# Performance work log

Hardware: AMD Instinct MI355X
Metric: run time of the kernel (lower is better)

## Reference

```python
import jax, jax.numpy as jnp
import numpy as np

N_NODES = 50000


def _gin_conv(x, src, dst, w1, b1, w2, b2):
    # sum-aggregate neighbor features: agg[i] = sum_{(j->i) in E} x[j]
    agg = jax.ops.segment_sum(x[src], dst, num_segments=N_NODES)
    h = x + agg  # eps = 0 (PyG GINConv default, not trainable)
    h = jnp.maximum(h @ w1 + b1, 0.0) @ w2 + b2
    return h


def setup_inputs() -> dict:
    key = jax.random.key(0)
    ks = jax.random.split(key, 10)
    d_in, d_h, d_out = 128, 256, 2
    E = 600000
    x = jax.random.normal(ks[0], (N_NODES, d_in), dtype=jnp.float32)
    edge_index = jax.random.randint(ks[1], (2, E), 0, N_NODES, dtype=jnp.int64)
    s = lambda k, sh: jax.random.normal(k, sh, dtype=jnp.float32) * (1.0 / np.sqrt(sh[0]))
    return {
        "x": x,
        "edge_index": edge_index,
        "w1": s(ks[2], (d_in, d_h)), "b1": jnp.zeros((d_h,), jnp.float32),
        "w2": s(ks[3], (d_h, d_h)), "b2": jnp.zeros((d_h,), jnp.float32),
        "w3": s(ks[4], (d_h, d_h)), "b3": jnp.zeros((d_h,), jnp.float32),
        "w4": s(ks[5], (d_h, d_out)), "b4": jnp.zeros((d_out,), jnp.float32),
    }


def reference(x, edge_index, w1, b1, w2, b2, w3, b3, w4, b4):
    src, dst = edge_index[0], edge_index[1]
    h = _gin_conv(x, src, dst, w1, b1, w2, b2)
    h = jnp.maximum(h, 0.0)  # F.relu between the two GINConv layers
    h = _gin_conv(h, src, dst, w3, b3, w4, b4)
    return jax.nn.log_softmax(h, axis=1)
```

## Files before the change

### kernel.cpp

```cpp
#include <hip/hip_runtime.h>
#include <hip/hip_bf16.h>


typedef __attribute__((ext_vector_type(8))) short bf16x8;
typedef __attribute__((ext_vector_type(4))) float f32x4;

static __device__ __forceinline__ unsigned short f2bf(float f) {
    unsigned int u = __float_as_uint(f);
    unsigned int r = (u + 0x7fffu + ((u >> 16) & 1u)) >> 16;
    return (unsigned short)r;
}
static __device__ __forceinline__ float bf2f(unsigned short s) {
    return __uint_as_float(((unsigned int)s) << 16);
}
static __device__ __forceinline__ float bflo(unsigned int u) {
    return __uint_as_float(u << 16);
}
static __device__ __forceinline__ float bfhi(unsigned int u) {
    return __uint_as_float(u & 0xffff0000u);
}

#define S1 136
#define S2 264

__global__ __launch_bounds__(256) void degree_kernel(
    const int* __restrict__ dst, int* __restrict__ deg, int E)
{
    const int e = blockIdx.x * 256 + threadIdx.x;
    if (e < E) atomicAdd(&deg[dst[e]], 1);
}

__global__ __launch_bounds__(256) void block_sum_kernel(
    const int* __restrict__ deg, int* __restrict__ bsum, int M)
{
    const int b = blockIdx.x, t = threadIdx.x;
    const int idx = b * 1024 + t * 4;
    int s = 0;
    if (idx + 3 < M) {
        const int4 v = *(const int4*)(deg + idx);
        s = v.x + v.y + v.z + v.w;
    } else {
        #pragma unroll
        for (int i = 0; i < 4; ++i) if (idx + i < M) s += deg[idx + i];
    }
    #pragma unroll
    for (int off = 32; off > 0; off >>= 1) s += __shfl_down(s, off);
    __shared__ int ws[4];
    if ((t & 63) == 0) ws[t >> 6] = s;
    __syncthreads();
    if (t == 0) bsum[b] = ws[0] + ws[1] + ws[2] + ws[3];
}

__global__ __launch_bounds__(64) void scan_partials_kernel(
    const int* __restrict__ bsum, int* __restrict__ boff, int nB)
{
    const int t = threadIdx.x;
    const int v = (t < nB) ? bsum[t] : 0;
    int inc = v;
    #pragma unroll
    for (int off = 1; off < 64; off <<= 1) {
        const int u = __shfl_up(inc, off);
        if (t >= off) inc += u;
    }
    if (t < nB) boff[t] = inc - v;
}

__global__ __launch_bounds__(256) void scan_blocks_kernel(
    const int* __restrict__ deg, const int* __restrict__ boff,
    int* __restrict__ rowptr, int* __restrict__ cur, int M, int E)
{
    const int b = blockIdx.x, t = threadIdx.x;
    const int idx = b * 1024 + t * 4;
    int4 d = make_int4(0, 0, 0, 0);
    if (idx + 3 < M) {
        d = *(const int4*)(deg + idx);
    } else {
        if (idx + 0 < M) d.x = deg[idx + 0];
        if (idx + 1 < M) d.y = deg[idx + 1];
        if (idx + 2 < M) d.z = deg[idx + 2];
        if (idx + 3 < M) d.w = deg[idx + 3];
    }
    const int tot = d.x + d.y + d.z + d.w;
    const int lane = t & 63, wid = t >> 6;
    int inc = tot;
    #pragma unroll
    for (int off = 1; off < 64; off <<= 1) {
        const int u = __shfl_up(inc, off);
        if (lane >= off) inc += u;
    }
    __shared__ int wsum[4];
    if (lane == 63) wsum[wid] = inc;
    __syncthreads();
    int woff = 0;
    #pragma unroll
    for (int w = 0; w < 4; ++w) if (w < wid) woff += wsum[w];
    int p = boff[b] + woff + (inc - tot);
    if (idx + 0 < M) { rowptr[idx + 0] = p; cur[idx + 0] = p; } p += d.x;
    if (idx + 1 < M) { rowptr[idx + 1] = p; cur[idx + 1] = p; } p += d.y;
    if (idx + 2 < M) { rowptr[idx + 2] = p; cur[idx + 2] = p; } p += d.z;
    if (idx + 3 < M) { rowptr[idx + 3] = p; cur[idx + 3] = p; }
    if (b == 0 && t == 0) rowptr[M] = E;
}

__global__ __launch_bounds__(256) void fill_kernel(
    const int* __restrict__ src, const int* __restrict__ dst,
    int* __restrict__ cur, int* __restrict__ srcs, int E)
{
    const int e = blockIdx.x * 256 + threadIdx.x;
    if (e >= E) return;
    const int p = atomicAdd(&cur[dst[e]], 1);
    srcs[p] = src[e];
}

__global__ __launch_bounds__(256) void cvt_bf16_kernel(
    const float* __restrict__ in, short* __restrict__ outb, int n4)
{
    const int i = (blockIdx.x * 256 + threadIdx.x);
    if (i >= n4) return;
    const float4 v = *(const float4*)(in + (size_t)i * 4);
    ushort4 o;
    o.x = f2bf(v.x); o.y = f2bf(v.y); o.z = f2bf(v.z); o.w = f2bf(v.w);
    *(ushort4*)(outb + (size_t)i * 4) = o;
}

__global__ __launch_bounds__(256) void transpose_cvt3_kernel(
    const float* __restrict__ w1, const float* __restrict__ w2, const float* __restrict__ w3,
    short* __restrict__ w1t, short* __restrict__ w2t, short* __restrict__ w3t)
{
    const int z = blockIdx.z;
    const float* in; short* outb; int K, ostride;
    if (z == 0)      { in = w1; outb = w1t; K = 128; ostride = S1; }
    else if (z == 1) { in = w2; outb = w2t; K = 256; ostride = S2; }
    else             { in = w3; outb = w3t; K = 256; ostride = S2; }
    const int N = 256;
    const int k0 = blockIdx.x * 32;
    if (k0 >= K) return;
    const int n0 = blockIdx.y * 32;
    __shared__ float tile[32][33];
    const int tx = threadIdx.x & 31;
    const int ty = threadIdx.x >> 5;
    #pragma unroll
    for (int i = 0; i < 4; ++i)
        tile[ty + 8 * i][tx] = in[(size_t)(k0 + ty + 8 * i) * N + n0 + tx];
    __syncthreads();
    #pragma unroll
    for (int i = 0; i < 4; ++i)
        outb[(size_t)(n0 + ty + 8 * i) * ostride + k0 + tx] = (short)f2bf(tile[tx][ty + 8 * i]);
}

__global__ __launch_bounds__(256) void gather_add_d128(
    const short* __restrict__ feat,
    const int* __restrict__ rowptr, const int* __restrict__ srcs,
    short* __restrict__ outb, int M)
{
    const int row = blockIdx.x * 4 + (threadIdx.x >> 6);
    if (row >= M) return;
    const int o = (threadIdx.x & 63) * 2;
    const unsigned int u = *(const unsigned int*)(feat + (size_t)row * 128 + o);
    float a0 = bflo(u), a1 = bfhi(u);
    const int jb = rowptr[row], je = rowptr[row + 1];
    int j = jb;
    for (; j + 8 <= je; j += 8) {
        unsigned int v[8];
        #pragma unroll
        for (int t = 0; t < 8; ++t) {
            const int s = srcs[j + t];
            v[t] = *(const unsigned int*)(feat + (size_t)s * 128 + o);
        }
        #pragma unroll
        for (int t = 0; t < 8; ++t) { a0 += bflo(v[t]); a1 += bfhi(v[t]); }
    }
    if (j + 4 <= je) {
        unsigned int v[4];
        #pragma unroll
        for (int t = 0; t < 4; ++t) {
            const int s = srcs[j + t];
            v[t] = *(const unsigned int*)(feat + (size_t)s * 128 + o);
        }
        #pragma unroll
        for (int t = 0; t < 4; ++t) { a0 += bflo(v[t]); a1 += bfhi(v[t]); }
        j += 4;
    }
    for (; j < je; ++j) {
        const unsigned int v = *(const unsigned int*)(feat + (size_t)srcs[j] * 128 + o);
        a0 += bflo(v); a1 += bfhi(v);
    }
    const unsigned int up = (unsigned int)f2bf(a0) | ((unsigned int)f2bf(a1) << 16);
    *(unsigned int*)(outb + (size_t)row * S1 + o) = up;
}

__global__ __launch_bounds__(256) void gather_add_d256(
    const short* __restrict__ feat,
    const int* __restrict__ rowptr, const int* __restrict__ srcs,
    short* __restrict__ outb, int M)
{
    const int row = blockIdx.x * 4 + (threadIdx.x >> 6);
    if (row >= M) return;
    const int o = (threadIdx.x & 63) * 4;
    const uint2 u = *(const uint2*)(feat + (size_t)row * 256 + o);
    float a0 = bflo(u.x), a1 = bfhi(u.x);
    float a2 = bflo(u.y), a3 = bfhi(u.y);
    const int jb = rowptr[row], je = rowptr[row + 1];
    int j = jb;
    for (; j + 8 <= je; j += 8) {
        uint2 v[8];
        #pragma unroll
        for (int t = 0; t < 8; ++t) {
            const int s = srcs[j + t];
            v[t] = *(const uint2*)(feat + (size_t)s * 256 + o);
        }
        #pragma unroll
        for (int t = 0; t < 8; ++t) {
            a0 += bflo(v[t].x); a1 += bfhi(v[t].x);
            a2 += bflo(v[t].y); a3 += bfhi(v[t].y);
        }
    }
    if (j + 4 <= je) {
        uint2 v[4];
        #pragma unroll
        for (int t = 0; t < 4; ++t) {
            const int s = srcs[j + t];
            v[t] = *(const uint2*)(feat + (size_t)s * 256 + o);
        }
        #pragma unroll
        for (int t = 0; t < 4; ++t) {
            a0 += bflo(v[t].x); a1 += bfhi(v[t].x);
            a2 += bflo(v[t].y); a3 += bfhi(v[t].y);
        }
        j += 4;
    }
    for (; j < je; ++j) {
        const uint2 v = *(const uint2*)(feat + (size_t)srcs[j] * 256 + o);
        a0 += bflo(v.x); a1 += bfhi(v.x); a2 += bflo(v.y); a3 += bfhi(v.y);
    }
    uint2 up;
    up.x = (unsigned int)f2bf(a0) | ((unsigned int)f2bf(a1) << 16);
    up.y = (unsigned int)f2bf(a2) | ((unsigned int)f2bf(a3) << 16);
    *(uint2*)(outb + (size_t)row * S2 + o) = up;
}

__global__ __launch_bounds__(256) void layer1_fused(
    const short* __restrict__ h1in,
    const short* __restrict__ w1t,
    const float* __restrict__ b1,
    const short* __restrict__ w2t,
    const float* __restrict__ b2,
    short* __restrict__ h1,
    int M)
{
    __shared__ short sT[64 * S2];
    const int tid  = threadIdx.x;
    const int lane = tid & 63;
    const int wid  = tid >> 6;
    const int r16  = lane & 15;
    const int q    = lane >> 4;
    const int tm   = blockIdx.x * 64;
    const int wn   = wid * 64;

    f32x4 acc[4][4];
    #pragma unroll
    for (int i = 0; i < 4; ++i)
        #pragma unroll
        for (int j = 0; j < 4; ++j)
            acc[i][j] = (f32x4)0.f;

    const short* Abase = h1in + (size_t)tm * S1;
    #pragma unroll
    for (int k0 = 0; k0 < 128; k0 += 32) {
        bf16x8 af[4], bfr[4];
        #pragma unroll
        for (int i = 0; i < 4; ++i)
            af[i] = *(const bf16x8*)(Abase + (size_t)(i * 16 + r16) * S1 + k0 + q * 8);
        #pragma unroll
        for (int j = 0; j < 4; ++j)
            bfr[j] = *(const bf16x8*)(w1t + (size_t)(wn + j * 16 + r16) * S1 + k0 + q * 8);
        #pragma unroll
        for (int i = 0; i < 4; ++i)
            #pragma unroll
            for (int j = 0; j < 4; ++j)
                acc[i][j] = __builtin_amdgcn_mfma_f32_16x16x32_bf16(af[i], bfr[j], acc[i][j], 0, 0, 0);
    }

    #pragma unroll
    for (int j = 0; j < 4; ++j) {
        const int col = wn + j * 16 + r16;
        const float bj = b1[col];
        #pragma unroll
        for (int i = 0; i < 4; ++i)
            #pragma unroll
            for (int r = 0; r < 4; ++r) {
                float v = fmaxf(acc[i][j][r] + bj, 0.f);
                sT[(i * 16 + q * 4 + r) * S2 + col] = (short)f2bf(v);
            }
    }
    __syncthreads();

    #pragma unroll
    for (int i = 0; i < 4; ++i)
        #pragma unroll
        for (int j = 0; j < 4; ++j)
            acc[i][j] = (f32x4)0.f;

    #pragma unroll
    for (int k0 = 0; k0 < 256; k0 += 32) {
        bf16x8 af[4], bfr[4];
        #pragma unroll
        for (int i = 0; i < 4; ++i)
            af[i] = *(const bf16x8*)(&sT[(i * 16 + r16) * S2 + k0 + q * 8]);
        #pragma unroll
        for (int j = 0; j < 4; ++j)
            bfr[j] = *(const bf16x8*)(w2t + (size_t)(wn + j * 16 + r16) * S2 + k0 + q * 8);
        #pragma unroll
        for (int i = 0; i < 4; ++i)
            #pragma unroll
            for (int j = 0; j < 4; ++j)
                acc[i][j] = __builtin_amdgcn_mfma_f32_16x16x32_bf16(af[i], bfr[j], acc[i][j], 0, 0, 0);
    }
    __syncthreads();

    #pragma unroll
    for (int j = 0; j < 4; ++j) {
        const int col = wn + j * 16 + r16;
        const float bj = b2[col];
        #pragma unroll
        for (int i = 0; i < 4; ++i)
            #pragma unroll
            for (int r = 0; r < 4; ++r) {
                float v = fmaxf(acc[i][j][r] + bj, 0.f);
                sT[(i * 16 + q * 4 + r) * S2 + col] = (short)f2bf(v);
            }
    }
    __syncthreads();

    #pragma unroll
    for (int c = 0; c < 8; ++c) {
        const int idx = tid + c * 256;
        const int row = idx >> 5;
        const int ch  = idx & 31;
        const int rg  = tm + row;
        if (rg < M) {
            const uint4 v = *(const uint4*)(&sT[row * S2 + ch * 8]);
            *(uint4*)(h1 + (size_t)rg * 256 + ch * 8) = v;
        }
    }
}

__global__ __launch_bounds__(256) void layer2_fused(
    const short* __restrict__ h2in,
    const short* __restrict__ w3t,
    const float* __restrict__ b3,
    const float* __restrict__ w4,
    const float* __restrict__ b4,
    float* __restrict__ out,
    int M)
{
    __shared__ short sT[64 * S2];
    const int tid  = threadIdx.x;
    const int lane = tid & 63;
    const int wid  = tid >> 6;
    const int r16  = lane & 15;
    const int q    = lane >> 4;
    const int tm   = blockIdx.x * 64;
    const int wn   = wid * 64;

    f32x4 acc[4][4];
    #pragma unroll
    for (int i = 0; i < 4; ++i)
        #pragma unroll
        for (int j = 0; j < 4; ++j)
            acc[i][j] = (f32x4)0.f;

    const short* Abase = h2in + (size_t)tm * S2;
    #pragma unroll
    for (int k0 = 0; k0 < 256; k0 += 32) {
        bf16x8 af[4], bfr[4];
        #pragma unroll
        for (int i = 0; i < 4; ++i)
            af[i] = *(const bf16x8*)(Abase + (size_t)(i * 16 + r16) * S2 + k0 + q * 8);
        #pragma unroll
        for (int j = 0; j < 4; ++j)
            bfr[j] = *(const bf16x8*)(w3t + (size_t)(wn + j * 16 + r16) * S2 + k0 + q * 8);
        #pragma unroll
        for (int i = 0; i < 4; ++i)
            #pragma unroll
            for (int j = 0; j < 4; ++j)
                acc[i][j] = __builtin_amdgcn_mfma_f32_16x16x32_bf16(af[i], bfr[j], acc[i][j], 0, 0, 0);
    }

    #pragma unroll
    for (int j = 0; j < 4; ++j) {
        const int col = wn + j * 16 + r16;
        const float bj = b3[col];
        #pragma unroll
        for (int i = 0; i < 4; ++i)
            #pragma unroll
            for (int r = 0; r < 4; ++r) {
                float v = fmaxf(acc[i][j][r] + bj, 0.f);
                sT[(i * 16 + q * 4 + r) * S2 + col] = (short)f2bf(v);
            }
    }
    __syncthreads();

    const int row = tid >> 2;
    const int qd  = tid & 3;
    const short* tp = &sT[row * S2 + qd * 64];
    const float* w4p = w4 + qd * 128;
    float s0 = 0.f, s1 = 0.f;
    #pragma unroll 8
    for (int k = 0; k < 64; ++k) {
        const float a = bf2f((unsigned short)tp[k]);
        const float2 w = *(const float2*)(w4p + 2 * k);
        s0 = fmaf(a, w.x, s0);
        s1 = fmaf(a, w.y, s1);
    }
    s0 += __shfl_down(s0, 2, 4);  s1 += __shfl_down(s1, 2, 4);
    s0 += __shfl_down(s0, 1, 4);  s1 += __shfl_down(s1, 1, 4);
    if (qd == 0) {
        const int rg = tm + row;
        if (rg < M) {
            s0 += b4[0];
            s1 += b4[1];
            const float m = fmaxf(s0, s1);
            const float l = logf(__expf(s0 - m) + __expf(s1 - m));
            float2 o;
            o.x = s0 - m - l;
            o.y = s1 - m - l;
            *(float2*)(out + (size_t)rg * 2) = o;
        }
    }
}

extern "C" void kernel_launch(void* const* d_in, const int* in_sizes, int n_in,
                              void* d_out, int out_size, void* d_ws, size_t ws_size,
                              hipStream_t stream)
{
    const float* x  = (const float*)d_in[0];
    const int*   ei = (const int*)d_in[1];
    const float* w1 = (const float*)d_in[2];
    const float* b1 = (const float*)d_in[3];
    const float* w2 = (const float*)d_in[4];
    const float* b2 = (const float*)d_in[5];
    const float* w3 = (const float*)d_in[6];
    const float* b3 = (const float*)d_in[7];
    const float* w4 = (const float*)d_in[8];
    const float* b4 = (const float*)d_in[9];

    const int DIN = 128, DH = 256;
    const int M = in_sizes[0] / DIN;
    const int E = in_sizes[1] / 2;
    const int* src = ei;
    const int* dst = ei + E;
    const int nB = (M + 1023) / 1024;

    int* deg    = (int*)d_ws;
    int* cur    = deg + M;
    int* rowptr = cur + M;
    int* bsum   = rowptr + (M + 1);
    int* boff   = bsum + 64;
    int* srcs   = boff + 64;
    size_t off = ((size_t)(3 * M + 1 + 128 + E) * sizeof(int) + 255) & ~(size_t)255;
    short* x_bf = (short*)((char*)d_ws + off);  off += (size_t)M * DIN * 2;
    off = (off + 255) & ~(size_t)255;
    short* h1in = (short*)((char*)d_ws + off);  off += (size_t)M * S1 * 2;
    off = (off + 255) & ~(size_t)255;
    short* h1   = (short*)((char*)d_ws + off);  off += (size_t)M * DH * 2;
    off = (off + 255) & ~(size_t)255;
    short* h2in = (short*)((char*)d_ws + off);  off += (size_t)M * S2 * 2;
    off = (off + 255) & ~(size_t)255;
    short* w1t  = (short*)((char*)d_ws + off);  off += (size_t)DH * S1 * 2;
    off = (off + 255) & ~(size_t)255;
    short* w2t  = (short*)((char*)d_ws + off);  off += (size_t)DH * S2 * 2;
    off = (off + 255) & ~(size_t)255;
    short* w3t  = (short*)((char*)d_ws + off);  off += (size_t)DH * S2 * 2;

    hipMemsetAsync(deg, 0, (size_t)M * sizeof(int), stream);
    degree_kernel<<<(E + 255) / 256, 256, 0, stream>>>(dst, deg, E);
    block_sum_kernel<<<nB, 256, 0, stream>>>(deg, bsum, M);
    scan_partials_kernel<<<1, 64, 0, stream>>>(bsum, boff, nB);
    scan_blocks_kernel<<<nB, 256, 0, stream>>>(deg, boff, rowptr, cur, M, E);
    fill_kernel<<<(E + 255) / 256, 256, 0, stream>>>(src, dst, cur, srcs, E);

    cvt_bf16_kernel<<<((M * DIN / 4) + 255) / 256, 256, 0, stream>>>(x, x_bf, M * DIN / 4);
    transpose_cvt3_kernel<<<dim3(8, 8, 3), 256, 0, stream>>>(w1, w2, w3, w1t, w2t, w3t);

    const int nblk = (M + 63) / 64;

    gather_add_d128<<<(M + 3) / 4, 256, 0, stream>>>(x_bf, rowptr, srcs, h1in, M);
    layer1_fused<<<nblk, 256, 0, stream>>>(h1in, w1t, b1, w2t, b2, h1, M);

    gather_add_d256<<<(M + 3) / 4, 256, 0, stream>>>(h1, rowptr, srcs, h2in, M);
    layer2_fused<<<nblk, 256, 0, stream>>>(h2in, w3t, b3, w4, b4, (float*)d_out, M);
}
```

Measured before the change: 289.0 us.

## Merge prep kernels, fold partial scan, and split gather across half-wavefronts

The memset, x-to-bf16 conversion and weight transpose are merged into one launch, and the block-offset scan is folded into the scan-blocks kernel, so the pipeline issues fewer kernel launches. Both gather kernels now split each wavefront into two halves that walk alternate neighbors with wider vector loads, then combine the halves with a cross-lane shuffle. This raises the number of neighbor loads in flight and the bytes per load, at the cost of extra registers and a reduction step. The new prep kernel's __syncthreads sits after early returns, but it only runs in the uniformly-branching transpose blocks.

```diff
diff --git a/kernel.cpp b/kernel.cpp
--- a/kernel.cpp
+++ b/kernel.cpp
@@ -22,6 +22,59 @@
 
 #define S1 136
 #define S2 264
+
+__global__ __launch_bounds__(256) void prep_kernel(
+    const float* __restrict__ x, short* __restrict__ x_bf,
+    const float* __restrict__ w1, const float* __restrict__ w2, const float* __restrict__ w3,
+    short* __restrict__ w1t, short* __restrict__ w2t, short* __restrict__ w3t,
+    int* __restrict__ deg, int M, int zB, int cB)
+{
+    const int b = blockIdx.x;
+    const int t = threadIdx.x;
+    if (b < zB) {
+        const int idx = b * 1024 + t * 4;
+        if (idx + 3 < M) {
+            *(int4*)(deg + idx) = make_int4(0, 0, 0, 0);
+        } else {
+            #pragma unroll
+            for (int i = 0; i < 4; ++i) if (idx + i < M) deg[idx + i] = 0;
+        }
+        return;
+    }
+    if (b < zB + cB) {
+        const int i = (b - zB) * 256 + t;
+        const int n4 = M * 32;
+        if (i >= n4) return;
+        const float4 v = *(const float4*)(x + (size_t)i * 4);
+        ushort4 o;
+        o.x = f2bf(v.x); o.y = f2bf(v.y); o.z = f2bf(v.z); o.w = f2bf(v.w);
+        *(ushort4*)(x_bf + (size_t)i * 4) = o;
+        return;
+    }
+    const int tb = b - zB - cB;
+    const int z = tb >> 6;
+    const int rem = tb & 63;
+    const int kb = rem & 7;
+    const int nb = rem >> 3;
+    const float* in; short* outb; int K, ostride;
+    if (z == 0)      { in = w1; outb = w1t; K = 128; ostride = S1; }
+    else if (z == 1) { in = w2; outb = w2t; K = 256; ostride = S2; }
+    else             { in = w3; outb = w3t; K = 256; ostride = S2; }
+    const int N = 256;
+    const int k0 = kb * 32;
+    if (k0 >= K) return;
+    const int n0 = nb * 32;
+    __shared__ float tile[32][33];
+    const int tx = t & 31;
+    const int ty = t >> 5;
+    #pragma unroll
+    for (int i = 0; i < 4; ++i)
+        tile[ty + 8 * i][tx] = in[(size_t)(k0 + ty + 8 * i) * N + n0 + tx];
+    __syncthreads();
+    #pragma unroll
+    for (int i = 0; i < 4; ++i)
+        outb[(size_t)(n0 + ty + 8 * i) * ostride + k0 + tx] = (short)f2bf(tile[tx][ty + 8 * i]);
+}
 
 __global__ __launch_bounds__(256) void degree_kernel(
     const int* __restrict__ dst, int* __restrict__ deg, int E)
@@ -51,25 +104,23 @@
     if (t == 0) bsum[b] = ws[0] + ws[1] + ws[2] + ws[3];
 }
 
-__global__ __launch_bounds__(64) void scan_partials_kernel(
-    const int* __restrict__ bsum, int* __restrict__ boff, int nB)
-{
-    const int t = threadIdx.x;
-    const int v = (t < nB) ? bsum[t] : 0;
-    int inc = v;
-    #pragma unroll
-    for (int off = 1; off < 64; off <<= 1) {
-        const int u = __shfl_up(inc, off);
-        if (t >= off) inc += u;
-    }
-    if (t < nB) boff[t] = inc - v;
-}
-
-__global__ __launch_bounds__(256) void scan_blocks_kernel(
-    const int* __restrict__ deg, const int* __restrict__ boff,
-    int* __restrict__ rowptr, int* __restrict__ cur, int M, int E)
+__global__ __launch_bounds__(256) void scan_blocks2_kernel(
+    const int* __restrict__ deg, const int* __restrict__ bsum,
+    int* __restrict__ rowptr, int* __restrict__ cur, int M, int E, int nB)
 {
     const int b = blockIdx.x, t = threadIdx.x;
+    __shared__ int sboff;
+    if (t < 64) {
+        const int v = (t < nB) ? bsum[t] : 0;
+        int inc = v;
+        #pragma unroll
+        for (int off = 1; off < 64; off <<= 1) {
+            const int u = __shfl_up(inc, off);
+            if (t >= off) inc += u;
+        }
+        const int prev = __shfl(inc, (b == 0) ? 0 : (b - 1));
+        if (t == 0) sboff = (b == 0) ? 0 : prev;
+    }
     const int idx = b * 1024 + t * 4;
     int4 d = make_int4(0, 0, 0, 0);
     if (idx + 3 < M) {
@@ -94,7 +145,7 @@
     int woff = 0;
     #pragma unroll
     for (int w = 0; w < 4; ++w) if (w < wid) woff += wsum[w];
-    int p = boff[b] + woff + (inc - tot);
+    int p = sboff + woff + (inc - tot);
     if (idx + 0 < M) { rowptr[idx + 0] = p; cur[idx + 0] = p; } p += d.x;
     if (idx + 1 < M) { rowptr[idx + 1] = p; cur[idx + 1] = p; } p += d.y;
     if (idx + 2 < M) { rowptr[idx + 2] = p; cur[idx + 2] = p; } p += d.z;
@@ -112,42 +163,6 @@
     srcs[p] = src[e];
 }
 
-__global__ __launch_bounds__(256) void cvt_bf16_kernel(
-    const float* __restrict__ in, short* __restrict__ outb, int n4)
-{
-    const int i = (blockIdx.x * 256 + threadIdx.x);
-    if (i >= n4) return;
-    const float4 v = *(const float4*)(in + (size_t)i * 4);
-    ushort4 o;
-    o.x = f2bf(v.x); o.y = f2bf(v.y); o.z = f2bf(v.z); o.w = f2bf(v.w);
-    *(ushort4*)(outb + (size_t)i * 4) = o;
-}
-
-__global__ __launch_bounds__(256) void transpose_cvt3_kernel(
-    const float* __restrict__ w1, const float* __restrict__ w2, const float* __restrict__ w3,
-    short* __restrict__ w1t, short* __restrict__ w2t, short* __restrict__ w3t)
-{
-    const int z = blockIdx.z;
-    const float* in; short* outb; int K, ostride;
-    if (z == 0)      { in = w1; outb = w1t; K = 128; ostride = S1; }
-    else if (z == 1) { in = w2; outb = w2t; K = 256; ostride = S2; }
-    else             { in = w3; outb = w3t; K = 256; ostride = S2; }
-    const int N = 256;
-    const int k0 = blockIdx.x * 32;
-    if (k0 >= K) return;
-    const int n0 = blockIdx.y * 32;
-    __shared__ float tile[32][33];
-    const int tx = threadIdx.x & 31;
-    const int ty = threadIdx.x >> 5;
-    #pragma unroll
-    for (int i = 0; i < 4; ++i)
-        tile[ty + 8 * i][tx] = in[(size_t)(k0 + ty + 8 * i) * N + n0 + tx];
-    __syncthreads();
-    #pragma unroll
-    for (int i = 0; i < 4; ++i)
-        outb[(size_t)(n0 + ty + 8 * i) * ostride + k0 + tx] = (short)f2bf(tile[tx][ty + 8 * i]);
-}
-
 __global__ __launch_bounds__(256) void gather_add_d128(
     const short* __restrict__ feat,
     const int* __restrict__ rowptr, const int* __restrict__ srcs,
@@ -155,38 +170,48 @@
 {
     const int row = blockIdx.x * 4 + (threadIdx.x >> 6);
     if (row >= M) return;
-    const int o = (threadIdx.x & 63) * 2;
-    const unsigned int u = *(const unsigned int*)(feat + (size_t)row * 128 + o);
-    float a0 = bflo(u), a1 = bfhi(u);
+    const int lane = threadIdx.x & 63;
+    const int half = lane >> 5;
+    const int o = (lane & 31) * 4;
+    float a0 = 0.f, a1 = 0.f, a2 = 0.f, a3 = 0.f;
+    if (half == 0) {
+        const uint2 u = *(const uint2*)(feat + (size_t)row * 128 + o);
+        a0 = bflo(u.x); a1 = bfhi(u.x); a2 = bflo(u.y); a3 = bfhi(u.y);
+    }
     const int jb = rowptr[row], je = rowptr[row + 1];
     int j = jb;
     for (; j + 8 <= je; j += 8) {
-        unsigned int v[8];
-        #pragma unroll
-        for (int t = 0; t < 8; ++t) {
-            const int s = srcs[j + t];
-            v[t] = *(const unsigned int*)(feat + (size_t)s * 128 + o);
-        }
-        #pragma unroll
-        for (int t = 0; t < 8; ++t) { a0 += bflo(v[t]); a1 += bfhi(v[t]); }
-    }
-    if (j + 4 <= je) {
-        unsigned int v[4];
+        uint2 v[4];
         #pragma unroll
         for (int t = 0; t < 4; ++t) {
-            const int s = srcs[j + t];
-            v[t] = *(const unsigned int*)(feat + (size_t)s * 128 + o);
-        }
-        #pragma unroll
-        for (int t = 0; t < 4; ++t) { a0 += bflo(v[t]); a1 += bfhi(v[t]); }
-        j += 4;
-    }
-    for (; j < je; ++j) {
-        const unsigned int v = *(const unsigned int*)(feat + (size_t)srcs[j] * 128 + o);
-        a0 += bflo(v); a1 += bfhi(v);
-    }
-    const unsigned int up = (unsigned int)f2bf(a0) | ((unsigned int)f2bf(a1) << 16);
-    *(unsigned int*)(outb + (size_t)row * S1 + o) = up;
+            const int s = srcs[j + 2 * t + half];
+            v[t] = *(const uint2*)(feat + (size_t)s * 128 + o);
+        }
+        #pragma unroll
+        for (int t = 0; t < 4; ++t) {
+            a0 += bflo(v[t].x); a1 += bfhi(v[t].x);
+            a2 += bflo(v[t].y); a3 += bfhi(v[t].y);
+        }
+    }
+    for (; j + 2 <= je; j += 2) {
+        const int s = srcs[j + half];
+        const uint2 v = *(const uint2*)(feat + (size_t)s * 128 + o);
+        a0 += bflo(v.x); a1 += bfhi(v.x); a2 += bflo(v.y); a3 += bfhi(v.y);
+    }
+    if (j < je && half == 0) {
+        const uint2 v = *(const uint2*)(feat + (size_t)srcs[j] * 128 + o);
+        a0 += bflo(v.x); a1 += bfhi(v.x); a2 += bflo(v.y); a3 += bfhi(v.y);
+    }
+    a0 += __shfl_down(a0, 32);
+    a1 += __shfl_down(a1, 32);
+    a2 += __shfl_down(a2, 32);
+    a3 += __shfl_down(a3, 32);
+    if (half == 0) {
+        uint2 up;
+        up.x = (unsigned int)f2bf(a0) | ((unsigned int)f2bf(a1) << 16);
+        up.y = (unsigned int)f2bf(a2) | ((unsigned int)f2bf(a3) << 16);
+        *(uint2*)(outb + (size_t)row * S1 + o) = up;
+    }
 }
 
 __global__ __launch_bounds__(256) void gather_add_d256(
@@ -196,47 +221,55 @@
 {
     const int row = blockIdx.x * 4 + (threadIdx.x >> 6);
     if (row >= M) return;
-    const int o = (threadIdx.x & 63) * 4;
-    const uint2 u = *(const uint2*)(feat + (size_t)row * 256 + o);
-    float a0 = bflo(u.x), a1 = bfhi(u.x);
-    float a2 = bflo(u.y), a3 = bfhi(u.y);
+    const int lane = threadIdx.x & 63;
+    const int half = lane >> 5;
+    const int o = (lane & 31) * 8;
+    float a[8];
+    #pragma unroll
+    for (int k = 0; k < 8; ++k) a[k] = 0.f;
+    if (half == 0) {
+        const uint4 u = *(const uint4*)(feat + (size_t)row * 256 + o);
+        a[0] = bflo(u.x); a[1] = bfhi(u.x); a[2] = bflo(u.y); a[3] = bfhi(u.y);
+        a[4] = bflo(u.z); a[5] = bfhi(u.z); a[6] = bflo(u.w); a[7] = bfhi(u.w);
+    }
     const int jb = rowptr[row], je = rowptr[row + 1];
     int j = jb;
     for (; j + 8 <= je; j += 8) {
-        uint2 v[8];
-        #pragma unroll
-        for (int t = 0; t < 8; ++t) {
-            const int s = srcs[j + t];
-            v[t] = *(const uint2*)(feat + (size_t)s * 256 + o);
-        }
-        #pragma unroll
-        for (int t = 0; t < 8; ++t) {
-            a0 += bflo(v[t].x); a1 += bfhi(v[t].x);
-            a2 += bflo(v[t].y); a3 += bfhi(v[t].y);
-        }
-    }
-    if (j + 4 <= je) {
-        uint2 v[4];
+        uint4 v[4];
         #pragma unroll
         for (int t = 0; t < 4; ++t) {
-            const int s = srcs[j + t];
-            v[t] = *(const uint2*)(feat + (size_t)s * 256 + o);
+            const int s = srcs[j + 2 * t + half];
+            v[t] = *(const uint4*)(feat + (size_t)s * 256 + o);
         }
         #pragma unroll
         for (int t = 0; t < 4; ++t) {
-            a0 += bflo(v[t].x); a1 += bfhi(v[t].x);
-            a2 += bflo(v[t].y); a3 += bfhi(v[t].y);
-        }
-        j += 4;
-    }
-    for (; j < je; ++j) {
-        const uint2 v = *(const uint2*)(feat + (size_t)srcs[j] * 256 + o);
-        a0 += bflo(v.x); a1 += bfhi(v.x); a2 += bflo(v.y); a3 += bfhi(v.y);
-    }
-    uint2 up;
-    up.x = (unsigned int)f2bf(a0) | ((unsigned int)f2bf(a1) << 16);
-    up.y = (unsigned int)f2bf(a2) | ((unsigned int)f2bf(a3) << 16);
-    *(uint2*)(outb + (size_t)row * S2 + o) = up;
+            a[0] += bflo(v[t].x); a[1] += bfhi(v[t].x);
+            a[2] += bflo(v[t].y); a[3] += bfhi(v[t].y);
+            a[4] += bflo(v[t].z); a[5] += bfhi(v[t].z);
+            a[6] += bflo(v[t].w); a[7] += bfhi(v[t].w);
+        }
+    }
+    for (; j + 2 <= je; j += 2) {
+        const int s = srcs[j + half];
+        const uint4 v = *(const uint4*)(feat + (size_t)s * 256 + o);
+        a[0] += bflo(v.x); a[1] += bfhi(v.x); a[2] += bflo(v.y); a[3] += bfhi(v.y);
+        a[4] += bflo(v.z); a[5] += bfhi(v.z); a[6] += bflo(v.w); a[7] += bfhi(v.w);
+    }
+    if (j < je && half == 0) {
+        const uint4 v = *(const uint4*)(feat + (size_t)srcs[j] * 256 + o);
+        a[0] += bflo(v.x); a[1] += bfhi(v.x); a[2] += bflo(v.y); a[3] += bfhi(v.y);
+        a[4] += bflo(v.z); a[5] += bfhi(v.z); a[6] += bflo(v.w); a[7] += bfhi(v.w);
+    }
+    #pragma unroll
+    for (int k = 0; k < 8; ++k) a[k] += __shfl_down(a[k], 32);
+    if (half == 0) {
+        uint4 up;
+        up.x = (unsigned int)f2bf(a[0]) | ((unsigned int)f2bf(a[1]) << 16);
+        up.y = (unsigned int)f2bf(a[2]) | ((unsigned int)f2bf(a[3]) << 16);
+        up.z = (unsigned int)f2bf(a[4]) | ((unsigned int)f2bf(a[5]) << 16);
+        up.w = (unsigned int)f2bf(a[6]) | ((unsigned int)f2bf(a[7]) << 16);
+        *(uint4*)(outb + (size_t)row * S2 + o) = up;
+    }
 }
 
 __global__ __launch_bounds__(256) void layer1_fused(
@@ -456,9 +489,8 @@
     int* cur    = deg + M;
     int* rowptr = cur + M;
     int* bsum   = rowptr + (M + 1);
-    int* boff   = bsum + 64;
-    int* srcs   = boff + 64;
-    size_t off = ((size_t)(3 * M + 1 + 128 + E) * sizeof(int) + 255) & ~(size_t)255;
+    int* srcs   = bsum + 64;
+    size_t off = ((size_t)(3 * M + 1 + 64 + E) * sizeof(int) + 255) & ~(size_t)255;
     short* x_bf = (short*)((char*)d_ws + off);  off += (size_t)M * DIN * 2;
     off = (off + 255) & ~(size_t)255;
     short* h1in = (short*)((char*)d_ws + off);  off += (size_t)M * S1 * 2;
@@ -473,15 +505,15 @@
     off = (off + 255) & ~(size_t)255;
     short* w3t  = (short*)((char*)d_ws + off);  off += (size_t)DH * S2 * 2;
 
-    hipMemsetAsync(deg, 0, (size_t)M * sizeof(int), stream);
+    const int zB = nB;
+    const int cB = (M * 32 + 255) / 256;
+    prep_kernel<<<zB + cB + 192, 256, 0, stream>>>(
+        x, x_bf, w1, w2, w3, w1t, w2t, w3t, deg, M, zB, cB);
+
     degree_kernel<<<(E + 255) / 256, 256, 0, stream>>>(dst, deg, E);
     block_sum_kernel<<<nB, 256, 0, stream>>>(deg, bsum, M);
-    scan_partials_kernel<<<1, 64, 0, stream>>>(bsum, boff, nB);
-    scan_blocks_kernel<<<nB, 256, 0, stream>>>(deg, boff, rowptr, cur, M, E);
+    scan_blocks2_kernel<<<nB, 256, 0, stream>>>(deg, bsum, rowptr, cur, M, E, nB);
     fill_kernel<<<(E + 255) / 256, 256, 0, stream>>>(src, dst, cur, srcs, E);
-
-    cvt_bf16_kernel<<<((M * DIN / 4) + 255) / 256, 256, 0, stream>>>(x, x_bf, M * DIN / 4);
-    transpose_cvt3_kernel<<<dim3(8, 8, 3), 256, 0, stream>>>(w1, w2, w3, w1t, w2t, w3t);
 
     const int nblk = (M + 63) / 64;
 
```

After: 285.1 us. No clear change (-1.4%).
